# Optimization experiments

Hardware: AMD Instinct MI355X
Metric: run time of the kernel (lower is better)

The kernel has to match this reference:

```python
import jax, jax.numpy as jnp
import numpy as np

PS = 4        # bkg_patch_size
PD = 1        # replicate pad
UFSTRIDE = 2  # patch-extraction stride
STRIDE = 1    # correlation stride
SCALE = 10.0  # softmax_scale


def pad_edge(x):
    return jnp.pad(x, ((0, 0), (0, 0), (PD, PD), (PD, PD)), mode='edge')


def unfold(x, ps, stride):
    # x: (B,C,H,W) -> (B, L, C, ps, ps), row-major over patch grid (matches F.unfold)
    B, C, H, W = x.shape
    oh = (H - ps) // stride + 1
    ow = (W - ps) // stride + 1
    ih = jnp.arange(oh)[:, None] * stride + jnp.arange(ps)[None, :]  # (oh, ps)
    iw = jnp.arange(ow)[:, None] * stride + jnp.arange(ps)[None, :]  # (ow, ps)
    p = x[:, :, ih][:, :, :, :, iw]            # (B,C,oh,ps,ow,ps)
    p = p.transpose(0, 2, 4, 1, 3, 5)          # (B,oh,ow,C,ps,ps)
    return p.reshape(B, oh * ow, C, ps, ps)


def diag3(x):
    # conv2d with 3x3 identity kernel, padding=1: out[i,j] = in[i-1,j-1]+in[i,j]+in[i+1,j+1]
    B, one, N, M = x.shape
    xp = jnp.pad(x, ((0, 0), (0, 0), (1, 1), (1, 1)))
    return xp[:, :, 0:N, 0:M] + xp[:, :, 1:N + 1, 1:M + 1] + xp[:, :, 2:N + 2, 2:M + 2]


def setup_inputs() -> dict:
    key = jax.random.key(0)
    k1, k2, k3 = jax.random.split(key, 3)
    B, C, H, W = 4, 64, 64, 64
    f = jax.random.normal(k1, (B, C, H, W), dtype=jnp.float32)
    b = jax.random.normal(k2, (B, C, H, W), dtype=jnp.float32)
    mask = (jax.random.uniform(k3, (B, 1, H, W)) < 0.25).astype(jnp.float32)
    return {"f": f, "b": b, "mask": mask}


def reference(f, b, mask):
    B, C, H, W = b.shape
    maskc = 1.0 - mask
    # --- get_conv_kernel: per-(batch,channel) L2-normalize b, extract patch kernels ---
    bn = b / jnp.sqrt(jnp.sum(b * b, axis=(2, 3), keepdims=True) + 1e-8)
    kernel = unfold(pad_edge(bn), PS, UFSTRIDE)                 # (B, L, C, ps, ps)
    mk = unfold(pad_edge(maskc), PS, UFSTRIDE)                  # (B, L, 1, ps, ps)
    mmk = jnp.mean(mk, axis=(2, 3, 4))[:, :, None, None]        # (B, L, 1, 1)
    L = kernel.shape[1]

    # --- batched grouped cross-correlation: conv f with per-sample patch kernels ---
    fpatch = unfold(pad_edge(f), PS, STRIDE)                    # (B, P, C, ps, ps)
    hs = (H + 2 * PD - PS) // STRIDE + 1
    ws = (W + 2 * PD - PS) // STRIDE + 1
    cos = jnp.einsum('bpcij,blcij->blp', fpatch, kernel)        # (B, L, P)
    cos = cos.reshape(B, L, hs, ws)

    # --- fuse: diagonal 3x3 convs along two axis pairings ---
    hb, wb = H // 2, W // 2
    cs = L
    c1 = diag3(cos.reshape(B, 1, cs, hs * ws))
    c1 = c1.reshape(B, 1, hb, wb, hs, ws).transpose(0, 1, 3, 2, 5, 4).reshape(B, 1, cs, hs * ws)
    c1 = diag3(c1)
    c1 = c1.reshape(B, 1, hb, wb, hs, ws).transpose(0, 1, 3, 2, 5, 4)
    cos = c1.reshape(B, cs, hs, ws)

    # --- irregular mask logic ---
    mp = unfold(pad_edge(maskc), PS, STRIDE)                    # (B, P, 1, ps, ps)
    mmp = jnp.mean(mp, axis=(2, 3, 4)).reshape(B, 1, hs, ws)    # (B, 1, hs, ws)
    mm = (mmk > mmp).astype(cos.dtype)                          # (B, L, hs, ws)
    ppp = (mmp > 0.5).astype(cos.dtype)
    mm = mm * ppp + (mmk == 1.0).astype(cos.dtype)
    mm = (mm > 0).astype(cos.dtype)

    cos = cos * mm
    return jax.nn.softmax(cos * SCALE, axis=1)
```

## Files before the change

### kernel.cpp

```cpp
#include <hip/hip_runtime.h>
#include <math.h>

#define NB 4
#define NC 64
#define NL 1024
#define NP 3969
#define PHW 63

typedef unsigned short ushort_t;
typedef __attribute__((ext_vector_type(8))) short short8;
typedef __attribute__((ext_vector_type(16))) float floatx16;

#define A_BSTRIDE 1048576
#define B_BSTRIDE 4128768

__global__ __launch_bounds__(256) void norm_kernel(const float* __restrict__ bsrc,
                                                   float* __restrict__ invn) {
    int bc = blockIdx.x;
    const float* src = bsrc + (size_t)bc * 4096;
    float s = 0.f;
    for (int i = threadIdx.x; i < 4096; i += 256) { float v = src[i]; s += v * v; }
#pragma unroll
    for (int off = 32; off > 0; off >>= 1) s += __shfl_down(s, off, 64);
    __shared__ float part[4];
    if ((threadIdx.x & 63) == 0) part[threadIdx.x >> 6] = s;
    __syncthreads();
    if (threadIdx.x == 0) {
        float t = part[0] + part[1] + part[2] + part[3];
        invn[bc] = 1.0f / sqrtf(t + 1e-8f);
    }
}

__global__ __launch_bounds__(256) void stats_kernel(const float* __restrict__ mask,
                                                    float* __restrict__ mmk,
                                                    float* __restrict__ mmp) {
    int id = blockIdx.x * 256 + threadIdx.x;
    if (id < NB * NL) {
        int b = id >> 10, l = id & 1023;
        int lh = l >> 5, lw = l & 31;
        const float* m = mask + b * 4096;
        float s = 0.f;
#pragma unroll
        for (int i = 0; i < 4; ++i) {
            int r = min(max(2 * lh - 1 + i, 0), 63);
#pragma unroll
            for (int j = 0; j < 4; ++j) {
                int c = min(max(2 * lw - 1 + j, 0), 63);
                s += 1.0f - m[r * 64 + c];
            }
        }
        mmk[id] = s * (1.0f / 16.0f);
    } else {
        int id2 = id - NB * NL;
        if (id2 < NB * NP) {
            int b = id2 / NP, p = id2 - b * NP;
            int ph = p / PHW, pw = p - ph * PHW;
            const float* m = mask + b * 4096;
            float s = 0.f;
#pragma unroll
            for (int i = 0; i < 4; ++i) {
                int r = min(max(ph - 1 + i, 0), 63);
#pragma unroll
                for (int j = 0; j < 4; ++j) {
                    int c = min(max(pw - 1 + j, 0), 63);
                    s += 1.0f - m[r * 64 + c];
                }
            }
            mmp[id2] = s * (1.0f / 16.0f);
        }
    }
}

__device__ inline void split_bf16(float v, ushort_t& hv, ushort_t& lv) {
    unsigned u = __float_as_uint(v);
    unsigned rr = u + 0x7FFFu + ((u >> 16) & 1u);
    hv = (ushort_t)(rr >> 16);
    float fh = __uint_as_float(((unsigned)hv) << 16);
    float remv = v - fh;
    unsigned u2 = __float_as_uint(remv);
    unsigned rr2 = u2 + 0x7FFFu + ((u2 >> 16) & 1u);
    lv = (ushort_t)(rr2 >> 16);
}

__device__ inline int frag_addr(int row, int kc) {
    return ((row >> 5) * 64 + kc) * 512 + (row & 31) * 8;
}

__global__ __launch_bounds__(256) void splitA_kernel(const float* __restrict__ bsrc,
                                                     const float* __restrict__ invn,
                                                     ushort_t* __restrict__ Ahi,
                                                     ushort_t* __restrict__ Alo) {
    __shared__ float fl[32 * 257];
    int lh = blockIdx.x, b = blockIdx.y, chalf = blockIdx.z;
    int t = threadIdx.x;
#pragma unroll
    for (int q = 0; q < 32; ++q) {
        int idx = t + (q << 8);
        int cl = idx >> 8, rem = idx & 255;
        int i = rem >> 6, s = rem & 63;
        int c = (chalf << 5) + cl;
        int r = min(max(2 * lh - 1 + i, 0), 63);
        fl[cl * 257 + rem] = bsrc[(((size_t)((b << 6) + c)) << 12) + (r << 6) + s];
    }
    __syncthreads();
    ushort_t* Ah = Ahi + (size_t)b * A_BSTRIDE;
    ushort_t* Al = Alo + (size_t)b * A_BSTRIDE;
#pragma unroll
    for (int q = 0; q < 4; ++q) {
        int pair = t + (q << 8);
        int lw = pair & 31, cl = pair >> 5;
        int c = (chalf << 5) + cl;
        float scale = invn[(b << 6) + c];
        const float* row = fl + cl * 257;
        __align__(16) ushort_t h[16];
        __align__(16) ushort_t lo[16];
#pragma unroll
        for (int i = 0; i < 4; ++i)
#pragma unroll
            for (int j = 0; j < 4; ++j) {
                int s = min(max(2 * lw - 1 + j, 0), 63);
                split_bf16(row[i * 64 + s] * scale, h[i * 4 + j], lo[i * 4 + j]);
            }
        int a = (lh * 64 + c) * 512 + lw * 8;
        *(uint4*)(Ah + a)       = *(uint4*)h;
        *(uint4*)(Ah + a + 256) = *(uint4*)(h + 8);
        *(uint4*)(Al + a)       = *(uint4*)lo;
        *(uint4*)(Al + a + 256) = *(uint4*)(lo + 8);
    }
}

__global__ __launch_bounds__(256) void splitB_kernel(const float* __restrict__ fsrc,
                                                     ushort_t* __restrict__ Bhi,
                                                     ushort_t* __restrict__ Blo) {
    __shared__ float fl[32 * 257];
    int ph = blockIdx.x, b = blockIdx.y, chalf = blockIdx.z;
    int t = threadIdx.x;
#pragma unroll
    for (int q = 0; q < 32; ++q) {
        int idx = t + (q << 8);
        int cl = idx >> 8, rem = idx & 255;
        int i = rem >> 6, s = rem & 63;
        int c = (chalf << 5) + cl;
        int r = min(max(ph - 1 + i, 0), 63);
        fl[cl * 257 + rem] = fsrc[(((size_t)((b << 6) + c)) << 12) + (r << 6) + s];
    }
    __syncthreads();
    ushort_t* Bh = Bhi + (size_t)b * B_BSTRIDE;
    ushort_t* Bl = Blo + (size_t)b * B_BSTRIDE;
#pragma unroll
    for (int q = 0; q < 8; ++q) {
        int pair = t + (q << 8);
        int pw = pair & 63, cl = pair >> 6;
        if (pw < PHW) {
            int c = (chalf << 5) + cl;
            const float* row = fl + cl * 257;
            __align__(16) ushort_t h[16];
            __align__(16) ushort_t lo[16];
#pragma unroll
            for (int i = 0; i < 4; ++i)
#pragma unroll
                for (int j = 0; j < 4; ++j) {
                    int s = min(max(pw - 1 + j, 0), 63);
                    split_bf16(row[i * 64 + s], h[i * 4 + j], lo[i * 4 + j]);
                }
            int p = ph * PHW + pw;
            int a = frag_addr(p, c);
            *(uint4*)(Bh + a)       = *(uint4*)h;
            *(uint4*)(Bh + a + 256) = *(uint4*)(h + 8);
            *(uint4*)(Bl + a)       = *(uint4*)lo;
            *(uint4*)(Bl + a + 256) = *(uint4*)(lo + 8);
        }
    }
    if (ph == 62) {
        uint4 z = {0, 0, 0, 0};
#pragma unroll
        for (int q = 0; q < 4; ++q) {
            int idx = t + (q << 8);
            int r31 = idx & 31, cl = idx >> 5;
            int c = (chalf << 5) + cl;
            if (r31 < 31) {
                int a = (124 * 64 + c) * 512 + (1 + r31) * 8;
                *(uint4*)(Bh + a) = z; *(uint4*)(Bh + a + 256) = z;
                *(uint4*)(Bl + a) = z; *(uint4*)(Bl + a + 256) = z;
            }
            int a2 = (125 * 64 + c) * 512 + r31 * 8;
            *(uint4*)(Bh + a2) = z; *(uint4*)(Bh + a2 + 256) = z;
            *(uint4*)(Bl + a2) = z; *(uint4*)(Bl + a2 + 256) = z;
        }
    }
}

__global__ __launch_bounds__(256, 2) void gemm_kernel(
    const ushort_t* __restrict__ Ahi, const ushort_t* __restrict__ Alo,
    const ushort_t* __restrict__ Bhi, const ushort_t* __restrict__ Blo,
    float* __restrict__ Rt) {
    int tid = threadIdx.x;
    int lane = tid & 63, w = tid >> 6;
    int bx = blockIdx.x;
    int b = blockIdx.y;
    int ltile = ((bx & 3) << 2) + w;
    int ptile = bx >> 2;
    int l0 = ltile << 6, p0 = ptile << 6;

    size_t la = (size_t)b * A_BSTRIDE + ((l0 >> 5) * 64) * 512 + lane * 8;
    size_t lb = (size_t)b * B_BSTRIDE + ((p0 >> 5) * 64) * 512 + lane * 8;
    const ushort_t* ah0 = Ahi + la;  const ushort_t* ah1 = ah0 + 32768;
    const ushort_t* al0 = Alo + la;  const ushort_t* al1 = al0 + 32768;
    const ushort_t* bh0 = Bhi + lb;  const ushort_t* bh1 = bh0 + 32768;
    const ushort_t* bl0 = Blo + lb;  const ushort_t* bl1 = bl0 + 32768;

    floatx16 acc[2][2];
#pragma unroll
    for (int i = 0; i < 2; ++i)
#pragma unroll
        for (int j = 0; j < 2; ++j)
#pragma unroll
            for (int r = 0; r < 16; ++r) acc[i][j][r] = 0.f;

    short8 f[4][8];

#define LOADC(dst, kc)                                   \
    do {                                                 \
        int o = (kc) * 512;                              \
        dst[0] = *(const short8*)(ah0 + o);              \
        dst[1] = *(const short8*)(ah1 + o);              \
        dst[2] = *(const short8*)(al0 + o);              \
        dst[3] = *(const short8*)(al1 + o);              \
        dst[4] = *(const short8*)(bh0 + o);              \
        dst[5] = *(const short8*)(bh1 + o);              \
        dst[6] = *(const short8*)(bl0 + o);              \
        dst[7] = *(const short8*)(bl1 + o);              \
    } while (0)

#define COMP(g)                                                                                       \
    do {                                                                                              \
        _Pragma("unroll")                                                                             \
        for (int pt = 0; pt < 2; ++pt)                                                                \
            _Pragma("unroll")                                                                         \
            for (int lt = 0; lt < 2; ++lt) {                                                          \
                acc[pt][lt] = __builtin_amdgcn_mfma_f32_32x32x16_bf16(g[4 + pt], g[0 + lt], acc[pt][lt], 0, 0, 0); \
                acc[pt][lt] = __builtin_amdgcn_mfma_f32_32x32x16_bf16(g[4 + pt], g[2 + lt], acc[pt][lt], 0, 0, 0); \
                acc[pt][lt] = __builtin_amdgcn_mfma_f32_32x32x16_bf16(g[6 + pt], g[0 + lt], acc[pt][lt], 0, 0, 0); \
            }                                                                                         \
    } while (0)

    LOADC(f[0], 0);
    LOADC(f[1], 1);
    LOADC(f[2], 2);
    for (int kc = 0; kc < 64; kc += 4) {
        LOADC(f[3], min(kc + 3, 63));
        COMP(f[0]);
        LOADC(f[0], min(kc + 4, 63));
        COMP(f[1]);
        LOADC(f[1], min(kc + 5, 63));
        COMP(f[2]);
        LOADC(f[2], min(kc + 6, 63));
        COMP(f[3]);
    }
#undef LOADC
#undef COMP

    int x = lane & 31, kg = lane >> 5;
#pragma unroll
    for (int pt = 0; pt < 2; ++pt)
#pragma unroll
        for (int lt = 0; lt < 2; ++lt)
#pragma unroll
            for (int r = 0; r < 16; ++r) {
                int p = p0 + (pt << 5) + (r & 3) + ((r >> 2) << 3) + (kg << 2);
                int l = l0 + (lt << 5) + x;
                if (p < NP) Rt[((size_t)b * NP + p) * NL + l] = acc[pt][lt][r];
            }
}

__global__ __launch_bounds__(256) void softmax_fused_kernel(const float* __restrict__ Rt,
                                                            const float* __restrict__ mmkA,
                                                            const float* __restrict__ mmpA,
                                                            float* __restrict__ E) {
    __shared__ float ld0[1024], ld1[1024], ld2[1024];
    __shared__ float red[8];
    int p = blockIdx.x, b = blockIdx.y;
    int ph = p / PHW, pw = p - ph * PHW;
    int t = threadIdx.x;
    int lane = t & 63, w = t >> 6;
    int l0 = t << 2;

    bool okm = (p != 0), okp = (p != 3968);
    int Pm = (ph > 0) ? p - 63 : 3905 + pw;
    int Pp = (ph < 62) ? p + 63 : pw + 1;

    const float* Rb = Rt + (size_t)b * NP * NL;
#define BUILD(dst, q)                                                   \
    do {                                                                \
        const float* base = Rb + (size_t)(q) * NL;                      \
        float4 r = *(const float4*)(base + l0);                         \
        if ((q) > 0) {                                                  \
            const float* pm = base - NL;                                \
            r.x += (l0 > 0) ? pm[l0 - 1] : 0.f;                         \
            r.y += pm[l0];  r.z += pm[l0 + 1];  r.w += pm[l0 + 2];      \
        }                                                               \
        if ((q) < NP - 1) {                                             \
            const float* pp = base + NL;                                \
            r.x += pp[l0 + 1];  r.y += pp[l0 + 2];  r.z += pp[l0 + 3];  \
            r.w += (l0 + 4 < NL) ? pp[l0 + 4] : 0.f;                    \
        }                                                               \
        *(float4*)(dst + l0) = r;                                       \
    } while (0)

    BUILD(ld0, p);
    if (okm) BUILD(ld1, Pm);
    if (okp) BUILD(ld2, Pp);
#undef BUILD
    __syncthreads();

    float4 vc = *(const float4*)(ld0 + l0);
    float4 vm = {0.f, 0.f, 0.f, 0.f}, vp = {0.f, 0.f, 0.f, 0.f};
    if (okm) {
        if (l0 >= 32) vm = *(const float4*)(ld1 + l0 - 32);
        else {
            vm.x = (l0 == 0) ? 0.f : ld1[l0 + 991];
            vm.y = ld1[l0 + 992];
            vm.z = ld1[l0 + 993];
            vm.w = ld1[l0 + 994];
        }
    }
    if (okp) {
        if (l0 < 992) vp = *(const float4*)(ld2 + l0 + 32);
        else {
            vp.x = ld2[l0 - 991];
            vp.y = ld2[l0 - 990];
            vp.z = ld2[l0 - 989];
            vp.w = (l0 + 3 == 1023) ? 0.f : ld2[l0 - 988];
        }
    }
    float mmpv = mmpA[b * NP + p];
    float4 km = *(const float4*)(mmkA + b * NL + l0);
    float lg[4];
    float fsum[4] = {vc.x + vm.x + vp.x, vc.y + vm.y + vp.y,
                     vc.z + vm.z + vp.z, vc.w + vm.w + vp.w};
    float kk[4] = {km.x, km.y, km.z, km.w};
#pragma unroll
    for (int i = 0; i < 4; ++i) {
        float mmv = (((kk[i] > mmpv) && (mmpv > 0.5f)) || (kk[i] == 1.0f)) ? 1.0f : 0.0f;
        lg[i] = fsum[i] * mmv * 10.0f;
    }
    float mx = fmaxf(fmaxf(lg[0], lg[1]), fmaxf(lg[2], lg[3]));
#pragma unroll
    for (int off = 32; off >= 1; off >>= 1) mx = fmaxf(mx, __shfl_xor(mx, off, 64));
    if (lane == 0) red[w] = mx;
    __syncthreads();
    mx = fmaxf(fmaxf(red[0], red[1]), fmaxf(red[2], red[3]));
    float e[4];
    float s = 0.f;
#pragma unroll
    for (int i = 0; i < 4; ++i) { e[i] = expf(lg[i] - mx); s += e[i]; }
#pragma unroll
    for (int off = 32; off >= 1; off >>= 1) s += __shfl_xor(s, off, 64);
    if (lane == 0) red[4 + w] = s;
    __syncthreads();
    float rinv = 1.0f / (red[4] + red[5] + red[6] + red[7]);
    float4 ev = {e[0] * rinv, e[1] * rinv, e[2] * rinv, e[3] * rinv};
    *(float4*)(E + (((size_t)b * NP + p) << 10) + l0) = ev;
}

__global__ __launch_bounds__(256) void transpose_kernel(const float* __restrict__ E,
                                                        float* __restrict__ out) {
    __shared__ float tile[63 * 65];
    int pt = blockIdx.x;
    int lt = blockIdx.y;
    int b  = blockIdx.z;
    int t = threadIdx.x;
    int p0 = pt * 63, l0 = lt << 6;
    const float* Eb = E + ((size_t)b * NP << 10);
    {
        int j = t & 63, i4 = t >> 6;
#pragma unroll
        for (int k = 0; k < 16; ++k) {
            int i = (k << 2) + i4;
            if (i < 63) tile[i * 65 + j] = Eb[((size_t)(p0 + i) << 10) + l0 + j];
        }
    }
    __syncthreads();
    {
        int ii = t & 63, jj4 = t >> 6;
        if (ii < 63) {
#pragma unroll
            for (int k = 0; k < 16; ++k) {
                int jj = (k << 2) + jj4;
                out[((size_t)b * NL + l0 + jj) * NP + p0 + ii] = tile[ii * 65 + jj];
            }
        }
    }
}

extern "C" void kernel_launch(void* const* d_in, const int* in_sizes, int n_in,
                              void* d_out, int out_size, void* d_ws, size_t ws_size,
                              hipStream_t stream) {
    const float* f    = (const float*)d_in[0];
    const float* b    = (const float*)d_in[1];
    const float* mask = (const float*)d_in[2];
    float* out = (float*)d_out;

    float* Rt = (float*)d_out;

    float* wsf = (float*)d_ws;
    float* E  = wsf + 16257024;
    ushort_t* Ahi = (ushort_t*)d_ws;
    ushort_t* Alo = Ahi + (size_t)NB * A_BSTRIDE;
    ushort_t* Bhi = Alo + (size_t)NB * A_BSTRIDE;
    ushort_t* Blo = Bhi + (size_t)NB * B_BSTRIDE;
    float* invn = wsf + 32514048;
    float* mmk = invn + 256;
    float* mmp = mmk + 4096;

    norm_kernel<<<dim3(256), dim3(256), 0, stream>>>(b, invn);
    stats_kernel<<<dim3(79), dim3(256), 0, stream>>>(mask, mmk, mmp);
    splitA_kernel<<<dim3(32, 4, 2), dim3(256), 0, stream>>>(b, invn, Ahi, Alo);
    splitB_kernel<<<dim3(63, 4, 2), dim3(256), 0, stream>>>(f, Bhi, Blo);
    gemm_kernel<<<dim3(252, 4), dim3(256), 0, stream>>>(Ahi, Alo, Bhi, Blo, Rt);
    softmax_fused_kernel<<<dim3(3969, 4), dim3(256), 0, stream>>>(Rt, mmk, mmp, E);
    transpose_kernel<<<dim3(63, 16, 4), dim3(256), 0, stream>>>(E, out);
}
```

Measured before the change: 295.0 us.

## Stage GEMM operands through LDS with double-buffered direct global-to-LDS loads

The bf16x3 split-precision GEMM is rewritten to use 512-thread blocks computing 256x256 output tiles. Operand fragments are staged into double-buffered shared memory with global_load_lds and shared by all eight waves, where before each wave read its own fragments from global memory. The B buffer is padded to a power-of-two stride so the zero tail can be cleared by a separate padB kernel. The aim is more operand reuse and less global traffic, at the cost of fewer, larger blocks (256 total), extra barriers, and one more kernel launch.

```diff
diff --git a/kernel.cpp b/kernel.cpp
--- a/kernel.cpp
+++ b/kernel.cpp
@@ -12,7 +12,7 @@
 typedef __attribute__((ext_vector_type(16))) float floatx16;
 
 #define A_BSTRIDE 1048576
-#define B_BSTRIDE 4128768
+#define B_BSTRIDE 4194304
 
 __global__ __launch_bounds__(256) void norm_kernel(const float* __restrict__ bsrc,
                                                    float* __restrict__ invn) {
@@ -127,6 +127,18 @@
         *(uint4*)(Al + a)       = *(uint4*)lo;
         *(uint4*)(Al + a + 256) = *(uint4*)(lo + 8);
     }
+}
+
+__global__ __launch_bounds__(256) void padB_kernel(ushort_t* __restrict__ Bhi,
+                                                   ushort_t* __restrict__ Blo) {
+    int idx = blockIdx.x * 256 + threadIdx.x;
+    int b = idx >> 15;
+    int r = idx & 32767;
+    int mat = r >> 14;
+    int o = r & 16383;
+    ushort_t* base = (mat ? Blo : Bhi) + (size_t)b * B_BSTRIDE + 124 * 32768;
+    uint4 z = {0u, 0u, 0u, 0u};
+    ((uint4*)base)[o] = z;
 }
 
 __global__ __launch_bounds__(256) void splitB_kernel(const float* __restrict__ fsrc,
@@ -171,104 +183,116 @@
             *(uint4*)(Bl + a + 256) = *(uint4*)(lo + 8);
         }
     }
-    if (ph == 62) {
-        uint4 z = {0, 0, 0, 0};
-#pragma unroll
-        for (int q = 0; q < 4; ++q) {
-            int idx = t + (q << 8);
-            int r31 = idx & 31, cl = idx >> 5;
-            int c = (chalf << 5) + cl;
-            if (r31 < 31) {
-                int a = (124 * 64 + c) * 512 + (1 + r31) * 8;
-                *(uint4*)(Bh + a) = z; *(uint4*)(Bh + a + 256) = z;
-                *(uint4*)(Bl + a) = z; *(uint4*)(Bl + a + 256) = z;
-            }
-            int a2 = (125 * 64 + c) * 512 + r31 * 8;
-            *(uint4*)(Bh + a2) = z; *(uint4*)(Bh + a2 + 256) = z;
-            *(uint4*)(Bl + a2) = z; *(uint4*)(Bl + a2 + 256) = z;
-        }
-    }
-}
-
-__global__ __launch_bounds__(256, 2) void gemm_kernel(
+}
+
+__global__ __launch_bounds__(512, 2) void gemm_kernel(
     const ushort_t* __restrict__ Ahi, const ushort_t* __restrict__ Alo,
     const ushort_t* __restrict__ Bhi, const ushort_t* __restrict__ Blo,
     float* __restrict__ Rt) {
+    __shared__ ushort_t smem[2][4][8][2][512];
     int tid = threadIdx.x;
     int lane = tid & 63, w = tid >> 6;
-    int bx = blockIdx.x;
-    int b = blockIdx.y;
-    int ltile = ((bx & 3) << 2) + w;
-    int ptile = bx >> 2;
-    int l0 = ltile << 6, p0 = ptile << 6;
-
-    size_t la = (size_t)b * A_BSTRIDE + ((l0 >> 5) * 64) * 512 + lane * 8;
-    size_t lb = (size_t)b * B_BSTRIDE + ((p0 >> 5) * 64) * 512 + lane * 8;
-    const ushort_t* ah0 = Ahi + la;  const ushort_t* ah1 = ah0 + 32768;
-    const ushort_t* al0 = Alo + la;  const ushort_t* al1 = al0 + 32768;
-    const ushort_t* bh0 = Bhi + lb;  const ushort_t* bh1 = bh0 + 32768;
-    const ushort_t* bl0 = Blo + lb;  const ushort_t* bl1 = bl0 + 32768;
-
-    floatx16 acc[2][2];
+    int wl = w >> 2, wp = w & 3;
+    int bx = blockIdx.x, b = blockIdx.y;
+    int L0 = (bx & 3) << 8;
+    int P0 = (bx >> 2) << 8;
+
+    int m = w >> 1;
+    int rt0 = (w & 1) << 2;
+    const ushort_t* gbase;
+    if (m == 0)      gbase = Ahi + (size_t)b * A_BSTRIDE + (size_t)(L0 >> 5) * 32768;
+    else if (m == 1) gbase = Alo + (size_t)b * A_BSTRIDE + (size_t)(L0 >> 5) * 32768;
+    else if (m == 2) gbase = Bhi + (size_t)b * B_BSTRIDE + (size_t)(P0 >> 5) * 32768;
+    else             gbase = Blo + (size_t)b * B_BSTRIDE + (size_t)(P0 >> 5) * 32768;
+    gbase += (size_t)(lane << 3);
+    int dst0 = ((((m << 3) + rt0) << 1)) * 512;
+
+    ushort_t* buf0 = &smem[0][0][0][0][0];
+    ushort_t* buf1 = &smem[1][0][0][0][0];
+
+#define STAGE(dstp, t)                                                                     \
+    do {                                                                                   \
+        int kb = (t) << 1;                                                                 \
+        _Pragma("unroll")                                                                  \
+        for (int j = 0; j < 4; ++j)                                                        \
+            _Pragma("unroll")                                                              \
+            for (int ks = 0; ks < 2; ++ks)                                                 \
+                __builtin_amdgcn_global_load_lds(                                          \
+                    (const __attribute__((address_space(1))) void*)(                       \
+                        gbase + (size_t)(rt0 + j) * 32768 + (size_t)(kb + ks) * 512),      \
+                    (__attribute__((address_space(3))) void*)(                             \
+                        (dstp) + dst0 + (((j << 1) + ks) * 512)),                          \
+                    16, 0, 0);                                                             \
+    } while (0)
+
+    floatx16 acc[2][4];
 #pragma unroll
     for (int i = 0; i < 2; ++i)
 #pragma unroll
-        for (int j = 0; j < 2; ++j)
+        for (int j = 0; j < 4; ++j)
 #pragma unroll
             for (int r = 0; r < 16; ++r) acc[i][j][r] = 0.f;
 
-    short8 f[4][8];
-
-#define LOADC(dst, kc)                                   \
-    do {                                                 \
-        int o = (kc) * 512;                              \
-        dst[0] = *(const short8*)(ah0 + o);              \
-        dst[1] = *(const short8*)(ah1 + o);              \
-        dst[2] = *(const short8*)(al0 + o);              \
-        dst[3] = *(const short8*)(al1 + o);              \
-        dst[4] = *(const short8*)(bh0 + o);              \
-        dst[5] = *(const short8*)(bh1 + o);              \
-        dst[6] = *(const short8*)(bl0 + o);              \
-        dst[7] = *(const short8*)(bl1 + o);              \
-    } while (0)
-
-#define COMP(g)                                                                                       \
-    do {                                                                                              \
-        _Pragma("unroll")                                                                             \
-        for (int pt = 0; pt < 2; ++pt)                                                                \
-            _Pragma("unroll")                                                                         \
-            for (int lt = 0; lt < 2; ++lt) {                                                          \
-                acc[pt][lt] = __builtin_amdgcn_mfma_f32_32x32x16_bf16(g[4 + pt], g[0 + lt], acc[pt][lt], 0, 0, 0); \
-                acc[pt][lt] = __builtin_amdgcn_mfma_f32_32x32x16_bf16(g[4 + pt], g[2 + lt], acc[pt][lt], 0, 0, 0); \
-                acc[pt][lt] = __builtin_amdgcn_mfma_f32_32x32x16_bf16(g[6 + pt], g[0 + lt], acc[pt][lt], 0, 0, 0); \
-            }                                                                                         \
-    } while (0)
-
-    LOADC(f[0], 0);
-    LOADC(f[1], 1);
-    LOADC(f[2], 2);
-    for (int kc = 0; kc < 64; kc += 4) {
-        LOADC(f[3], min(kc + 3, 63));
-        COMP(f[0]);
-        LOADC(f[0], min(kc + 4, 63));
-        COMP(f[1]);
-        LOADC(f[1], min(kc + 5, 63));
-        COMP(f[2]);
-        LOADC(f[2], min(kc + 6, 63));
-        COMP(f[3]);
-    }
-#undef LOADC
-#undef COMP
+    STAGE(buf0, 0);
+    ushort_t* cur = buf0;
+    ushort_t* nxt = buf1;
+
+    int aoff = (wl << 2) * 1024;
+    int boff = 16384 + (wp << 1) * 1024;
+
+    for (int t = 0; t < 32; ++t) {
+        asm volatile("" ::: "memory");
+        __builtin_amdgcn_s_barrier();
+        asm volatile("" ::: "memory");
+        if (t < 31) {
+            STAGE(nxt, t + 1);
+            asm volatile("s_waitcnt vmcnt(8)" ::: "memory");
+        } else {
+            asm volatile("s_waitcnt vmcnt(0)" ::: "memory");
+        }
+        __builtin_amdgcn_s_barrier();
+        asm volatile("" ::: "memory");
+
+        const ushort_t* rb = cur + (lane << 3);
+#pragma unroll
+        for (int ks = 0; ks < 2; ++ks) {
+            short8 ah[4], al[4], bh[2], bl[2];
+#pragma unroll
+            for (int lt = 0; lt < 4; ++lt) {
+                ah[lt] = *(const short8*)(rb + aoff + lt * 1024 + ks * 512);
+                al[lt] = *(const short8*)(rb + 8192 + aoff + lt * 1024 + ks * 512);
+            }
+#pragma unroll
+            for (int pt = 0; pt < 2; ++pt) {
+                bh[pt] = *(const short8*)(rb + boff + pt * 1024 + ks * 512);
+                bl[pt] = *(const short8*)(rb + 8192 + boff + pt * 1024 + ks * 512);
+            }
+            __builtin_amdgcn_s_setprio(1);
+#pragma unroll
+            for (int pt = 0; pt < 2; ++pt)
+#pragma unroll
+                for (int lt = 0; lt < 4; ++lt) {
+                    acc[pt][lt] = __builtin_amdgcn_mfma_f32_32x32x16_bf16(bh[pt], ah[lt], acc[pt][lt], 0, 0, 0);
+                    acc[pt][lt] = __builtin_amdgcn_mfma_f32_32x32x16_bf16(bh[pt], al[lt], acc[pt][lt], 0, 0, 0);
+                    acc[pt][lt] = __builtin_amdgcn_mfma_f32_32x32x16_bf16(bl[pt], ah[lt], acc[pt][lt], 0, 0, 0);
+                }
+            __builtin_amdgcn_s_setprio(0);
+        }
+        ushort_t* tmp = cur; cur = nxt; nxt = tmp;
+    }
+#undef STAGE
 
     int x = lane & 31, kg = lane >> 5;
+    int pw0 = P0 + (wp << 6);
+    int lw0 = L0 + (wl << 7);
 #pragma unroll
     for (int pt = 0; pt < 2; ++pt)
 #pragma unroll
-        for (int lt = 0; lt < 2; ++lt)
+        for (int lt = 0; lt < 4; ++lt)
 #pragma unroll
             for (int r = 0; r < 16; ++r) {
-                int p = p0 + (pt << 5) + (r & 3) + ((r >> 2) << 3) + (kg << 2);
-                int l = l0 + (lt << 5) + x;
+                int p = pw0 + (pt << 5) + (r & 3) + ((r >> 2) << 3) + (kg << 2);
+                int l = lw0 + (lt << 5) + x;
                 if (p < NP) Rt[((size_t)b * NP + p) * NL + l] = acc[pt][lt][r];
             }
 }
@@ -416,8 +440,9 @@
     norm_kernel<<<dim3(256), dim3(256), 0, stream>>>(b, invn);
     stats_kernel<<<dim3(79), dim3(256), 0, stream>>>(mask, mmk, mmp);
     splitA_kernel<<<dim3(32, 4, 2), dim3(256), 0, stream>>>(b, invn, Ahi, Alo);
+    padB_kernel<<<dim3(512), dim3(256), 0, stream>>>(Bhi, Blo);
     splitB_kernel<<<dim3(63, 4, 2), dim3(256), 0, stream>>>(f, Bhi, Blo);
-    gemm_kernel<<<dim3(252, 4), dim3(256), 0, stream>>>(Ahi, Alo, Bhi, Blo, Rt);
+    gemm_kernel<<<dim3(64, 4), dim3(512), 0, stream>>>(Ahi, Alo, Bhi, Blo, Rt);
     softmax_fused_kernel<<<dim3(3969, 4), dim3(256), 0, stream>>>(Rt, mmk, mmp, E);
     transpose_kernel<<<dim3(63, 16, 4), dim3(256), 0, stream>>>(E, out);
 }
```

New measurement: 269.8 us. 8.6% less time.
